# Performance work log

Hardware: AMD Instinct MI355X
Metric: run time of the kernel (lower is better)

Reference implementation:

```python
import jax, jax.numpy as jnp
import numpy as np

NUM_NODES = 10000
NUM_FEAT = 32
HIDDEN = 64
OUT_FEAT = 16
NUM_EDGES = 160000
SEQ_LEN = 12
BATCH = 1


def _gcn_conv(x, W, b, row, col, n):
    # PyG GCNConv: h = D^-1/2 (A+I) D^-1/2 (x @ W) + b
    # x: (n, T, F_in), row/col: (E+n,) with self-loops already appended
    h = x @ W                                              # (n, T, H)
    deg = jax.ops.segment_sum(jnp.ones_like(col, dtype=h.dtype), col, num_segments=n)
    dis = 1.0 / jnp.sqrt(jnp.maximum(deg, 1.0))            # deg >= 1 due to self-loops
    norm = dis[row] * dis[col]                             # (E+n,)
    msg = h[row] * norm[:, None, None]                     # gather + scale
    return jax.ops.segment_sum(msg, col, num_segments=n) + b


def _lstm_layer(x, wih, whh, bih, bhh):
    # x: (N, T, F); PyTorch gate order i, f, g, o
    H = whh.shape[1]
    Nn = x.shape[0]
    bias = bih + bhh

    def step(carry, xt):
        h, c = carry
        g = xt @ wih.T + h @ whh.T + bias
        i, f, gg, o = jnp.split(g, 4, axis=-1)
        c = jax.nn.sigmoid(f) * c + jax.nn.sigmoid(i) * jnp.tanh(gg)
        h = jax.nn.sigmoid(o) * jnp.tanh(c)
        return (h, c), h

    h0 = jnp.zeros((Nn, H), x.dtype)
    c0 = jnp.zeros((Nn, H), x.dtype)
    _, ys = jax.lax.scan(step, (h0, c0), jnp.transpose(x, (1, 0, 2)))
    return jnp.transpose(ys, (1, 0, 2))                    # (N, T, H)


def setup_inputs() -> dict:
    key = jax.random.key(0)
    ks = jax.random.split(key, 16)
    s_in = 1.0 / np.sqrt(NUM_FEAT)
    s_h = 1.0 / np.sqrt(HIDDEN)
    inp = {
        "x": jax.random.normal(ks[0], (BATCH, SEQ_LEN, NUM_NODES, NUM_FEAT), jnp.float32),
        "edge_index": jax.random.randint(ks[1], (2, NUM_EDGES), 0, NUM_NODES, dtype=jnp.int64),
        "gw0": jax.random.normal(ks[2], (NUM_FEAT, HIDDEN), jnp.float32) * s_in,
        "gb0": jnp.zeros((HIDDEN,), jnp.float32),
        "gw1": jax.random.normal(ks[3], (HIDDEN, HIDDEN), jnp.float32) * s_h,
        "gb1": jnp.zeros((HIDDEN,), jnp.float32),
        "wih0": jax.random.normal(ks[4], (4 * HIDDEN, HIDDEN), jnp.float32) * s_h,
        "whh0": jax.random.normal(ks[5], (4 * HIDDEN, HIDDEN), jnp.float32) * s_h,
        "bih0": jax.random.normal(ks[6], (4 * HIDDEN,), jnp.float32) * s_h,
        "bhh0": jax.random.normal(ks[7], (4 * HIDDEN,), jnp.float32) * s_h,
        "wih1": jax.random.normal(ks[8], (4 * HIDDEN, HIDDEN), jnp.float32) * s_h,
        "whh1": jax.random.normal(ks[9], (4 * HIDDEN, HIDDEN), jnp.float32) * s_h,
        "bih1": jax.random.normal(ks[10], (4 * HIDDEN,), jnp.float32) * s_h,
        "bhh1": jax.random.normal(ks[11], (4 * HIDDEN,), jnp.float32) * s_h,
        "fc_w": jax.random.normal(ks[12], (OUT_FEAT, HIDDEN), jnp.float32) * s_h,
        "fc_b": jnp.zeros((OUT_FEAT,), jnp.float32),
    }
    return inp


def reference(x, edge_index, gw0, gb0, gw1, gb1, wih0, whh0, bih0, bhh0,
              wih1, whh1, bih1, bhh1, fc_w, fc_b):
    B, T, n, F = x.shape
    BN = B * n
    # (B, T, N, F) -> (B, N, T, F) -> (B*N, T, F); the per-timestep GCN loop in
    # the original is batched over T here (same math, edge_index is time-invariant).
    xs = jnp.transpose(x, (0, 2, 1, 3)).reshape(BN, T, F)
    loops = jnp.arange(BN, dtype=edge_index.dtype)
    row = jnp.concatenate([edge_index[0], loops])
    col = jnp.concatenate([edge_index[1], loops])
    h = jax.nn.relu(_gcn_conv(xs, gw0, gb0, row, col, BN))
    h = jax.nn.relu(_gcn_conv(h, gw1, gb1, row, col, BN))
    h = _lstm_layer(h, wih0, whh0, bih0, bhh0)
    h = _lstm_layer(h, wih1, whh1, bih1, bhh1)
    out = h[:, -1, :] @ fc_w.T + fc_b                      # last timestep only
    return out.reshape(B, n, OUT_FEAT)
```

## Files before the change

kernel.cpp:

```cpp
#include <hip/hip_runtime.h>
#include <hip/hip_bf16.h>

constexpr int kNN  = 10000;
constexpr int kTT  = 12;
constexpr int kFIN = 32;
constexpr int kHH  = 64;
constexpr int kH4  = 256;
constexpr int kOUT = 16;
constexpr int kNE  = 160000;

typedef _Float16 half8 __attribute__((ext_vector_type(8)));
typedef _Float16 half4 __attribute__((ext_vector_type(4)));
typedef _Float16 half2t __attribute__((ext_vector_type(2)));
typedef float floatx4 __attribute__((ext_vector_type(4)));

__device__ __forceinline__ float sigf(float x){ return 1.f/(1.f+__expf(-x)); }
__device__ __forceinline__ float tanh_fast(float x){
  float xc = fminf(fmaxf(x,-30.f),30.f);
  float e = __expf(-2.f*xc);
  return (1.f-e)/(1.f+e);
}

__global__ void k_detect(const int* __restrict__ ei, int* __restrict__ anyf){
  int a = 0;
  for (int i = blockIdx.x*256 + threadIdx.x; i < kNE; i += gridDim.x*256)
    a |= ei[2*i+1];
  unsigned long long m = __ballot(a != 0);
  if ((threadIdx.x & 63) == 0 && m) atomicOr(anyf, 1);
}

__global__ void k_deg(const int* __restrict__ ei, const int* __restrict__ anyf,
                      int* __restrict__ cnt){
  int e = blockIdx.x*256 + threadIdx.x;
  if (e >= kNE) return;
  int c = (anyf[0]==0) ? ei[2*(kNE+e)] : ei[kNE+e];
  atomicAdd(&cnt[c], 1);
}

__global__ void k_scan(const int* __restrict__ cnt, int* __restrict__ offs,
                       float* __restrict__ dis){
  __shared__ int part[256];
  int tid = threadIdx.x;
  const int CH = (kNN + 255)/256;
  int lo = tid*CH, hi = min(lo+CH, kNN);
  int s = 0;
  for (int i = lo; i < hi; ++i) s += cnt[i];
  part[tid] = s;
  __syncthreads();
  if (tid == 0){
    int run = 0;
    for (int i = 0; i < 256; ++i){ int v = part[i]; part[i] = run; run += v; }
  }
  __syncthreads();
  int run = part[tid];
  for (int i = lo; i < hi; ++i){ offs[i] = run; run += cnt[i]; }
  if (hi == kNN) offs[kNN] = run;
  for (int i = tid; i < kNN; i += 256) dis[i] = rsqrtf((float)(cnt[i]+1));
}

__global__ void k_scatter(const int* __restrict__ ei, const int* __restrict__ anyf,
                          const int* __restrict__ offs, int* __restrict__ cur,
                          const float* __restrict__ dis,
                          int* __restrict__ esrc, float* __restrict__ ew){
  int e = blockIdx.x*256 + threadIdx.x;
  if (e >= kNE) return;
  int f = (anyf[0]==0);
  int r = f ? ei[2*e]         : ei[e];
  int c = f ? ei[2*(kNE+e)]   : ei[kNE+e];
  int p = offs[c] + atomicAdd(&cur[c], 1);
  esrc[p] = r;
  ew[p] = dis[r]*dis[c];
}

template<int K, int N, typename TI>
__global__ __launch_bounds__(256) void k_gemm(const TI* __restrict__ in,
                      const float* __restrict__ Wg,
                      _Float16* __restrict__ out){
  constexpr int COLG = N/4;
  constexpr int ROWG = 256/COLG;
  constexpr int MR   = 4;
  constexpr int MTILE= ROWG*MR;
  constexpr int AP   = K + 4;
  __shared__ float Wl[K*N];
  __shared__ float Al[MTILE*AP];
  int tid = threadIdx.x;
  int m0 = blockIdx.x*MTILE;
  if constexpr (__is_same(TI, _Float16)){
    for (int idx = tid; idx < MTILE*K/8; idx += 256){
      int r = idx/(K/8), k8 = idx - r*(K/8);
      half8 v = *(const half8*)&in[(size_t)(m0 + r)*K + k8*8];
      float* dst = &Al[r*AP + k8*8];
      #pragma unroll
      for (int j = 0; j < 8; ++j) dst[j] = (float)v[j];
    }
  } else {
    for (int idx = tid; idx < MTILE*K/4; idx += 256){
      int r = idx/(K/4), k4 = idx - r*(K/4);
      float4 v = *(const float4*)&in[(size_t)(m0 + r)*K + k4*4];
      float* dst = &Al[r*AP + k4*4];
      dst[0]=v.x; dst[1]=v.y; dst[2]=v.z; dst[3]=v.w;
    }
  }
  for (int idx = tid; idx < K*N; idx += 256) Wl[idx] = Wg[idx];
  __syncthreads();
  int cg = tid % COLG, rg = tid / COLG;
  int c0 = cg*4, r0 = rg*MR;
  float acc[MR][4];
  #pragma unroll
  for (int r=0;r<MR;++r){acc[r][0]=0.f;acc[r][1]=0.f;acc[r][2]=0.f;acc[r][3]=0.f;}
  #pragma unroll 2
  for (int k = 0; k < K; k += 4){
    float4 wv[4];
    #pragma unroll
    for (int kk = 0; kk < 4; ++kk) wv[kk] = *(const float4*)&Wl[(k+kk)*N + c0];
    #pragma unroll
    for (int r = 0; r < MR; ++r){
      float4 a4 = *(const float4*)&Al[(r0+r)*AP + k];
      acc[r][0] = fmaf(a4.x, wv[0].x, acc[r][0]);
      acc[r][1] = fmaf(a4.x, wv[0].y, acc[r][1]);
      acc[r][2] = fmaf(a4.x, wv[0].z, acc[r][2]);
      acc[r][3] = fmaf(a4.x, wv[0].w, acc[r][3]);
      acc[r][0] = fmaf(a4.y, wv[1].x, acc[r][0]);
      acc[r][1] = fmaf(a4.y, wv[1].y, acc[r][1]);
      acc[r][2] = fmaf(a4.y, wv[1].z, acc[r][2]);
      acc[r][3] = fmaf(a4.y, wv[1].w, acc[r][3]);
      acc[r][0] = fmaf(a4.z, wv[2].x, acc[r][0]);
      acc[r][1] = fmaf(a4.z, wv[2].y, acc[r][1]);
      acc[r][2] = fmaf(a4.z, wv[2].z, acc[r][2]);
      acc[r][3] = fmaf(a4.z, wv[2].w, acc[r][3]);
      acc[r][0] = fmaf(a4.w, wv[3].x, acc[r][0]);
      acc[r][1] = fmaf(a4.w, wv[3].y, acc[r][1]);
      acc[r][2] = fmaf(a4.w, wv[3].z, acc[r][2]);
      acc[r][3] = fmaf(a4.w, wv[3].w, acc[r][3]);
    }
  }
  #pragma unroll
  for (int r = 0; r < MR; ++r){
    half4 hv;
    hv[0]=(_Float16)acc[r][0]; hv[1]=(_Float16)acc[r][1];
    hv[2]=(_Float16)acc[r][2]; hv[3]=(_Float16)acc[r][3];
    *(half4*)&out[(size_t)(m0 + r0 + r)*N + c0] = hv;
  }
}

template<bool TM>
__global__ __launch_bounds__(256) void k_agg(const _Float16* __restrict__ hin,
                     _Float16* __restrict__ hout,
                     const float* __restrict__ bias, const float* __restrict__ dis,
                     const int* __restrict__ offs, const int* __restrict__ esrc,
                     const float* __restrict__ ew){
  int wid = threadIdx.x >> 6, lane = threadIdx.x & 63;
  int gw = blockIdx.x*4 + wid;
  int tp = gw / kNN, n = gw - tp*kNN;
  int sel = lane >> 5, fp = lane & 31;
  int t = 2*tp + sel;
  const _Float16* hb = hin + (size_t)t*kNN*kHH;
  float d = dis[n], ws = d*d;
  half2t sv = *(const half2t*)&hb[(size_t)n*kHH + 2*fp];
  float a0 = ws*(float)sv[0], a1 = ws*(float)sv[1];
  int e0 = offs[n], e1 = offs[n+1];
  int e = e0;
  for (; e + 8 <= e1; e += 8){
    int s[8]; float w[8];
    #pragma unroll
    for (int u = 0; u < 8; ++u){ s[u] = esrc[e+u]; w[u] = ew[e+u]; }
    half2t v[8];
    #pragma unroll
    for (int u = 0; u < 8; ++u) v[u] = *(const half2t*)&hb[(size_t)s[u]*kHH + 2*fp];
    #pragma unroll
    for (int u = 0; u < 8; ++u){
      a0 = fmaf(w[u], (float)v[u][0], a0);
      a1 = fmaf(w[u], (float)v[u][1], a1);
    }
  }
  for (; e < e1; ++e){
    int su = esrc[e]; float wu = ew[e];
    half2t vu = *(const half2t*)&hb[(size_t)su*kHH + 2*fp];
    a0 = fmaf(wu, (float)vu[0], a0);
    a1 = fmaf(wu, (float)vu[1], a1);
  }
  a0 = fmaxf(a0 + bias[2*fp],   0.f);
  a1 = fmaxf(a1 + bias[2*fp+1], 0.f);
  half2t o; o[0] = (_Float16)a0; o[1] = (_Float16)a1;
  size_t oi = TM ? ((size_t)t*kNN + n)*kHH + 2*fp
                 : ((size_t)n*kTT + t)*kHH + 2*fp;
  *(half2t*)&hout[oi] = o;
}

__global__ __launch_bounds__(512) void k_rec2(const _Float16* __restrict__ xin,
                     const float* __restrict__ wih0, const float* __restrict__ whh0,
                     const float* __restrict__ bih0, const float* __restrict__ bhh0,
                     const float* __restrict__ wih1, const float* __restrict__ whh1,
                     const float* __restrict__ bih1, const float* __restrict__ bhh1,
                     const float* __restrict__ fcw, const float* __restrict__ fcb,
                     float* __restrict__ out){
  constexpr int LP = 72;
  __shared__ _Float16 h0b[2][16*LP];
  __shared__ _Float16 h1b[2][16*LP];
  int tid = threadIdx.x, w = tid >> 6, lane = tid & 63;
  int lo = lane & 15, hi4 = lane >> 4;
  int layer = w >> 2, wl = w & 3;
  int nb = blockIdx.x*16;

  const float* wih = layer ? wih1 : wih0;
  const float* whh = layer ? whh1 : whh0;
  const float* bi_ = layer ? bih1 : bih0;
  const float* bh_ = layer ? bhh1 : bhh0;

  half8 BI[4][2], BH[4][2];
  #pragma unroll
  for (int q = 0; q < 4; ++q){
    int row = q*kHH + wl*16 + lo;
    #pragma unroll
    for (int kt = 0; kt < 2; ++kt){
      const float* pi = wih + (size_t)row*kHH + kt*32 + hi4*8;
      const float* ph = whh + (size_t)row*kHH + kt*32 + hi4*8;
      half8 fi, fh;
      #pragma unroll
      for (int j = 0; j < 8; ++j){ fi[j] = (_Float16)pi[j]; fh[j] = (_Float16)ph[j]; }
      BI[q][kt] = fi; BH[q][kt] = fh;
    }
  }
  float bias[4];
  #pragma unroll
  for (int q = 0; q < 4; ++q){
    int col = q*kHH + wl*16 + lo;
    bias[q] = bi_[col] + bh_[col];
  }
  half8 FW[2];
  if (w == 4){
    #pragma unroll
    for (int kt = 0; kt < 2; ++kt){
      const float* pf = fcw + (size_t)lo*kHH + kt*32 + hi4*8;
      half8 f;
      #pragma unroll
      for (int j = 0; j < 8; ++j) f[j] = (_Float16)pf[j];
      FW[kt] = f;
    }
  }

  float c[4] = {0.f,0.f,0.f,0.f};
  half8 ax[2], ah[2], axn[2];

  const _Float16* xrow = xin + (size_t)(nb + lo)*kTT*kHH;
  if (layer == 0){
    #pragma unroll
    for (int kt = 0; kt < 2; ++kt) axn[kt] = *(const half8*)&xrow[kt*32 + hi4*8];
  }

  for (int i = 0; i < 13; ++i){
    int t = layer ? i-1 : i;
    bool act = layer ? (i >= 1) : (i < 12);
    if (act){
      if (layer == 0){
        ax[0] = axn[0]; ax[1] = axn[1];
        if (t < kTT-1){
          #pragma unroll
          for (int kt = 0; kt < 2; ++kt)
            axn[kt] = *(const half8*)&xrow[(size_t)(t+1)*kHH + kt*32 + hi4*8];
        }
      }
      floatx4 acc[4];
      #pragma unroll
      for (int q = 0; q < 4; ++q){
        floatx4 a = {0.f,0.f,0.f,0.f};
        a = __builtin_amdgcn_mfma_f32_16x16x32_f16(ax[0], BI[q][0], a, 0,0,0);
        a = __builtin_amdgcn_mfma_f32_16x16x32_f16(ax[1], BI[q][1], a, 0,0,0);
        acc[q] = a;
      }
      if (t > 0){
        #pragma unroll
        for (int q = 0; q < 4; ++q){
          floatx4 a = acc[q];
          a = __builtin_amdgcn_mfma_f32_16x16x32_f16(ah[0], BH[q][0], a, 0,0,0);
          a = __builtin_amdgcn_mfma_f32_16x16x32_f16(ah[1], BH[q][1], a, 0,0,0);
          acc[q] = a;
        }
      }
      _Float16* hb = layer ? &h1b[t & 1][0] : &h0b[t & 1][0];
      #pragma unroll
      for (int r = 0; r < 4; ++r){
        float gi = acc[0][r] + bias[0];
        float gf = acc[1][r] + bias[1];
        float gg = acc[2][r] + bias[2];
        float go = acc[3][r] + bias[3];
        float ii = sigf(gi), ff = sigf(gf), gt = tanh_fast(gg), oo = sigf(go);
        c[r] = ff*c[r] + ii*gt;
        float hn = oo * tanh_fast(c[r]);
        hb[(hi4*4 + r)*LP + wl*16 + lo] = (_Float16)hn;
      }
    }
    __syncthreads();
    if (layer == 0){
      if (i < 11){
        const _Float16* rb = &h0b[i & 1][0];
        #pragma unroll
        for (int kt = 0; kt < 2; ++kt)
          ah[kt] = *(const half8*)&rb[lo*LP + kt*32 + hi4*8];
      }
    } else {
      if (i < 12){
        const _Float16* rb = &h0b[i & 1][0];
        #pragma unroll
        for (int kt = 0; kt < 2; ++kt)
          ax[kt] = *(const half8*)&rb[lo*LP + kt*32 + hi4*8];
      }
      if (i >= 1 && i < 12){
        const _Float16* rb = &h1b[(i-1) & 1][0];
        #pragma unroll
        for (int kt = 0; kt < 2; ++kt)
          ah[kt] = *(const half8*)&rb[lo*LP + kt*32 + hi4*8];
      }
    }
  }
  if (w == 4){
    const _Float16* rb = &h1b[1][0];
    half8 a0 = *(const half8*)&rb[lo*LP + 0*32 + hi4*8];
    half8 a1 = *(const half8*)&rb[lo*LP + 1*32 + hi4*8];
    floatx4 a = {0.f,0.f,0.f,0.f};
    a = __builtin_amdgcn_mfma_f32_16x16x32_f16(a0, FW[0], a, 0,0,0);
    a = __builtin_amdgcn_mfma_f32_16x16x32_f16(a1, FW[1], a, 0,0,0);
    float bo = fcb[lo];
    #pragma unroll
    for (int r = 0; r < 4; ++r)
      out[(size_t)(nb + hi4*4 + r)*kOUT + lo] = a[r] + bo;
  }
}

extern "C" void kernel_launch(void* const* d_in, const int* in_sizes, int n_in,
                              void* d_out, int out_size, void* d_ws, size_t ws_size,
                              hipStream_t stream){
  const float* x    = (const float*)d_in[0];
  const int*   ei   = (const int*)  d_in[1];
  const float* gw0  = (const float*)d_in[2];
  const float* gb0  = (const float*)d_in[3];
  const float* gw1  = (const float*)d_in[4];
  const float* gb1  = (const float*)d_in[5];
  const float* wih0 = (const float*)d_in[6];
  const float* whh0 = (const float*)d_in[7];
  const float* bih0 = (const float*)d_in[8];
  const float* bhh0 = (const float*)d_in[9];
  const float* wih1 = (const float*)d_in[10];
  const float* whh1 = (const float*)d_in[11];
  const float* bih1 = (const float*)d_in[12];
  const float* bhh1 = (const float*)d_in[13];
  const float* fcw  = (const float*)d_in[14];
  const float* fcb  = (const float*)d_in[15];
  float* out = (float*)d_out;

  char* ws = (char*)d_ws;
  size_t p = 0;
  auto carve = [&](size_t bytes)->char*{
    char* r = ws + p;
    p += (bytes + 255) & ~(size_t)255;
    return r;
  };
  int*   anyf = (int*)  carve(256);
  int*   cnt  = (int*)  carve(sizeof(int)*kNN);
  int*   cur  = (int*)  carve(sizeof(int)*kNN);
  size_t zbytes = p;
  int*   offs = (int*)  carve(sizeof(int)*(kNN+1));
  float* dis  = (float*)carve(sizeof(float)*kNN);
  int*   esrc = (int*)  carve(sizeof(int)*kNE);
  float* ew   = (float*)carve(sizeof(float)*kNE);
  _Float16* bufA = (_Float16*)carve(sizeof(_Float16)*(size_t)kNN*kTT*kHH);
  _Float16* bufB = (_Float16*)carve(sizeof(_Float16)*(size_t)kNN*kTT*kHH);
  (void)ws_size; (void)in_sizes; (void)n_in; (void)out_size;

  hipMemsetAsync(ws, 0, zbytes, stream);
  k_detect <<<80, 256, 0, stream>>>(ei, anyf);
  k_deg    <<<(kNE+255)/256, 256, 0, stream>>>(ei, anyf, cnt);
  k_scan   <<<1, 256, 0, stream>>>(cnt, offs, dis);
  k_scatter<<<(kNE+255)/256, 256, 0, stream>>>(ei, anyf, offs, cur, dis, esrc, ew);

  k_gemm<kFIN, kHH, float><<<(kNN*kTT)/64, 256, 0, stream>>>(x, gw0, bufA);
  k_agg<true> <<<(kNN*kTT/2)/4, 256, 0, stream>>>(bufA, bufB, gb0, dis, offs, esrc, ew);
  k_gemm<kHH, kHH, _Float16><<<(kNN*kTT)/64, 256, 0, stream>>>(bufB, gw1, bufA);
  k_agg<false><<<(kNN*kTT/2)/4, 256, 0, stream>>>(bufA, bufB, gb1, dis, offs, esrc, ew);

  k_rec2<<<kNN/16, 512, 0, stream>>>(bufB, wih0, whh0, bih0, bhh0,
                                     wih1, whh1, bih1, bhh1, fcw, fcb, out);
}
```

Measured before the change: 343.4 us.

## Aggregate before transform in GCN, pack edge data, batch two tiles per LSTM block

Several changes land together. The first GCN layer now aggregates the 32-wide input before the matmul, which uses the linearity of A(XW) = (AX)W to cut gather width. Bias and ReLU move into the GEMM epilogue. Edge source and weight are packed into one int2, and the edge bounds are made wave-uniform with readfirstlane. Input x is cast to fp16 inside the detect kernel, the scan uses wave shuffles, and the LSTM kernel handles two 16-node tiles per block to amortise weight loads and sync. The risks are an extra fp16 rounding of x and fewer LSTM blocks (313), which lowers occupancy across CUs.

After: 328.3 us. 4.4% less time.

```diff
diff --git a/kernel.cpp b/kernel.cpp
--- a/kernel.cpp
+++ b/kernel.cpp
@@ -21,12 +21,20 @@
   return (1.f-e)/(1.f+e);
 }
 
-__global__ void k_detect(const int* __restrict__ ei, int* __restrict__ anyf){
+__global__ void k_detect_cast(const int* __restrict__ ei, int* __restrict__ anyf,
+                              const float* __restrict__ x, _Float16* __restrict__ xh){
   int a = 0;
   for (int i = blockIdx.x*256 + threadIdx.x; i < kNE; i += gridDim.x*256)
     a |= ei[2*i+1];
   unsigned long long m = __ballot(a != 0);
   if ((threadIdx.x & 63) == 0 && m) atomicOr(anyf, 1);
+  const int NV = kNN*kTT*kFIN/4;
+  for (int i = blockIdx.x*256 + threadIdx.x; i < NV; i += gridDim.x*256){
+    float4 v = *(const float4*)&x[4*i];
+    half4 h;
+    h[0]=(_Float16)v.x; h[1]=(_Float16)v.y; h[2]=(_Float16)v.z; h[3]=(_Float16)v.w;
+    *(half4*)&xh[4*i] = h;
+  }
 }
 
 __global__ void k_deg(const int* __restrict__ ei, const int* __restrict__ anyf,
@@ -39,20 +47,24 @@
 
 __global__ void k_scan(const int* __restrict__ cnt, int* __restrict__ offs,
                        float* __restrict__ dis){
-  __shared__ int part[256];
+  __shared__ int wsum[4];
   int tid = threadIdx.x;
   const int CH = (kNN + 255)/256;
   int lo = tid*CH, hi = min(lo+CH, kNN);
   int s = 0;
   for (int i = lo; i < hi; ++i) s += cnt[i];
-  part[tid] = s;
+  int orig = s;
+  int lane = tid & 63, wv = tid >> 6;
+  #pragma unroll
+  for (int d = 1; d < 64; d <<= 1){
+    int v = __shfl_up(s, d, 64);
+    if (lane >= d) s += v;
+  }
+  if (lane == 63) wsum[wv] = s;
   __syncthreads();
-  if (tid == 0){
-    int run = 0;
-    for (int i = 0; i < 256; ++i){ int v = part[i]; part[i] = run; run += v; }
-  }
-  __syncthreads();
-  int run = part[tid];
+  int add = 0;
+  for (int k2 = 0; k2 < wv; ++k2) add += wsum[k2];
+  int run = s - orig + add;
   for (int i = lo; i < hi; ++i){ offs[i] = run; run += cnt[i]; }
   if (hi == kNN) offs[kNN] = run;
   for (int i = tid; i < kNN; i += 256) dis[i] = rsqrtf((float)(cnt[i]+1));
@@ -61,20 +73,63 @@
 __global__ void k_scatter(const int* __restrict__ ei, const int* __restrict__ anyf,
                           const int* __restrict__ offs, int* __restrict__ cur,
                           const float* __restrict__ dis,
-                          int* __restrict__ esrc, float* __restrict__ ew){
+                          int2* __restrict__ edat){
   int e = blockIdx.x*256 + threadIdx.x;
   if (e >= kNE) return;
   int f = (anyf[0]==0);
   int r = f ? ei[2*e]         : ei[e];
   int c = f ? ei[2*(kNE+e)]   : ei[kNE+e];
   int p = offs[c] + atomicAdd(&cur[c], 1);
-  esrc[p] = r;
-  ew[p] = dis[r]*dis[c];
-}
-
-template<int K, int N, typename TI>
-__global__ __launch_bounds__(256) void k_gemm(const TI* __restrict__ in,
-                      const float* __restrict__ Wg,
+  edat[p] = make_int2(r, __float_as_int(dis[r]*dis[c]));
+}
+
+template<int F>
+__global__ __launch_bounds__(256) void k_agg(const _Float16* __restrict__ hin,
+                     _Float16* __restrict__ hout,
+                     const float* __restrict__ dis,
+                     const int* __restrict__ offs, const int2* __restrict__ edat){
+  constexpr int LPF = F/2;
+  constexpr int TPW = 64/LPF;
+  int wid = threadIdx.x >> 6, lane = threadIdx.x & 63;
+  int gw = blockIdx.x*4 + wid;
+  int tq = gw / kNN, n = gw - tq*kNN;
+  int fp = lane & (LPF-1), tsub = lane / LPF;
+  int t = TPW*tq + tsub;
+  const _Float16* hb = hin + (size_t)t*kNN*F;
+  float d = dis[n], ws = d*d;
+  half2t sv = *(const half2t*)&hb[(size_t)n*F + 2*fp];
+  float a0 = ws*(float)sv[0], a1 = ws*(float)sv[1];
+  int e0 = __builtin_amdgcn_readfirstlane(offs[n]);
+  int e1 = __builtin_amdgcn_readfirstlane(offs[n+1]);
+  int e = e0;
+  for (; e + 8 <= e1; e += 8){
+    int2 d8[8];
+    #pragma unroll
+    for (int u = 0; u < 8; ++u) d8[u] = edat[e+u];
+    half2t v[8];
+    #pragma unroll
+    for (int u = 0; u < 8; ++u) v[u] = *(const half2t*)&hb[(size_t)d8[u].x*F + 2*fp];
+    #pragma unroll
+    for (int u = 0; u < 8; ++u){
+      float wu = __int_as_float(d8[u].y);
+      a0 = fmaf(wu, (float)v[u][0], a0);
+      a1 = fmaf(wu, (float)v[u][1], a1);
+    }
+  }
+  for (; e < e1; ++e){
+    int2 du = edat[e];
+    float wu = __int_as_float(du.y);
+    half2t vu = *(const half2t*)&hb[(size_t)du.x*F + 2*fp];
+    a0 = fmaf(wu, (float)vu[0], a0);
+    a1 = fmaf(wu, (float)vu[1], a1);
+  }
+  half2t o; o[0] = (_Float16)a0; o[1] = (_Float16)a1;
+  *(half2t*)&hout[((size_t)t*kNN + n)*F + 2*fp] = o;
+}
+
+template<int K, int N, bool NM>
+__global__ __launch_bounds__(256) void k_gemm(const _Float16* __restrict__ in,
+                      const float* __restrict__ Wg, const float* __restrict__ bias,
                       _Float16* __restrict__ out){
   constexpr int COLG = N/4;
   constexpr int ROWG = 256/COLG;
@@ -85,21 +140,12 @@
   __shared__ float Al[MTILE*AP];
   int tid = threadIdx.x;
   int m0 = blockIdx.x*MTILE;
-  if constexpr (__is_same(TI, _Float16)){
-    for (int idx = tid; idx < MTILE*K/8; idx += 256){
-      int r = idx/(K/8), k8 = idx - r*(K/8);
-      half8 v = *(const half8*)&in[(size_t)(m0 + r)*K + k8*8];
-      float* dst = &Al[r*AP + k8*8];
-      #pragma unroll
-      for (int j = 0; j < 8; ++j) dst[j] = (float)v[j];
-    }
-  } else {
-    for (int idx = tid; idx < MTILE*K/4; idx += 256){
-      int r = idx/(K/4), k4 = idx - r*(K/4);
-      float4 v = *(const float4*)&in[(size_t)(m0 + r)*K + k4*4];
-      float* dst = &Al[r*AP + k4*4];
-      dst[0]=v.x; dst[1]=v.y; dst[2]=v.z; dst[3]=v.w;
-    }
+  for (int idx = tid; idx < MTILE*K/8; idx += 256){
+    int r = idx/(K/8), k8 = idx - r*(K/8);
+    half8 v = *(const half8*)&in[(size_t)(m0 + r)*K + k8*8];
+    float* dst = &Al[r*AP + k8*8];
+    #pragma unroll
+    for (int j = 0; j < 8; ++j) dst[j] = (float)v[j];
   }
   for (int idx = tid; idx < K*N; idx += 256) Wl[idx] = Wg[idx];
   __syncthreads();
@@ -134,57 +180,20 @@
       acc[r][3] = fmaf(a4.w, wv[3].w, acc[r][3]);
     }
   }
+  float4 bb = *(const float4*)&bias[c0];
   #pragma unroll
   for (int r = 0; r < MR; ++r){
     half4 hv;
-    hv[0]=(_Float16)acc[r][0]; hv[1]=(_Float16)acc[r][1];
-    hv[2]=(_Float16)acc[r][2]; hv[3]=(_Float16)acc[r][3];
-    *(half4*)&out[(size_t)(m0 + r0 + r)*N + c0] = hv;
-  }
-}
-
-template<bool TM>
-__global__ __launch_bounds__(256) void k_agg(const _Float16* __restrict__ hin,
-                     _Float16* __restrict__ hout,
-                     const float* __restrict__ bias, const float* __restrict__ dis,
-                     const int* __restrict__ offs, const int* __restrict__ esrc,
-                     const float* __restrict__ ew){
-  int wid = threadIdx.x >> 6, lane = threadIdx.x & 63;
-  int gw = blockIdx.x*4 + wid;
-  int tp = gw / kNN, n = gw - tp*kNN;
-  int sel = lane >> 5, fp = lane & 31;
-  int t = 2*tp + sel;
-  const _Float16* hb = hin + (size_t)t*kNN*kHH;
-  float d = dis[n], ws = d*d;
-  half2t sv = *(const half2t*)&hb[(size_t)n*kHH + 2*fp];
-  float a0 = ws*(float)sv[0], a1 = ws*(float)sv[1];
-  int e0 = offs[n], e1 = offs[n+1];
-  int e = e0;
-  for (; e + 8 <= e1; e += 8){
-    int s[8]; float w[8];
-    #pragma unroll
-    for (int u = 0; u < 8; ++u){ s[u] = esrc[e+u]; w[u] = ew[e+u]; }
-    half2t v[8];
-    #pragma unroll
-    for (int u = 0; u < 8; ++u) v[u] = *(const half2t*)&hb[(size_t)s[u]*kHH + 2*fp];
-    #pragma unroll
-    for (int u = 0; u < 8; ++u){
-      a0 = fmaf(w[u], (float)v[u][0], a0);
-      a1 = fmaf(w[u], (float)v[u][1], a1);
-    }
-  }
-  for (; e < e1; ++e){
-    int su = esrc[e]; float wu = ew[e];
-    half2t vu = *(const half2t*)&hb[(size_t)su*kHH + 2*fp];
-    a0 = fmaf(wu, (float)vu[0], a0);
-    a1 = fmaf(wu, (float)vu[1], a1);
-  }
-  a0 = fmaxf(a0 + bias[2*fp],   0.f);
-  a1 = fmaxf(a1 + bias[2*fp+1], 0.f);
-  half2t o; o[0] = (_Float16)a0; o[1] = (_Float16)a1;
-  size_t oi = TM ? ((size_t)t*kNN + n)*kHH + 2*fp
-                 : ((size_t)n*kTT + t)*kHH + 2*fp;
-  *(half2t*)&hout[oi] = o;
+    hv[0]=(_Float16)fmaxf(acc[r][0]+bb.x, 0.f);
+    hv[1]=(_Float16)fmaxf(acc[r][1]+bb.y, 0.f);
+    hv[2]=(_Float16)fmaxf(acc[r][2]+bb.z, 0.f);
+    hv[3]=(_Float16)fmaxf(acc[r][3]+bb.w, 0.f);
+    int m = m0 + r0 + r;
+    size_t oi;
+    if (NM){ int t = m/kNN, n = m - t*kNN; oi = ((size_t)n*kTT + t)*N + c0; }
+    else    oi = (size_t)m*N + c0;
+    *(half4*)&out[oi] = hv;
+  }
 }
 
 __global__ __launch_bounds__(512) void k_rec2(const _Float16* __restrict__ xin,
@@ -195,12 +204,12 @@
                      const float* __restrict__ fcw, const float* __restrict__ fcb,
                      float* __restrict__ out){
   constexpr int LP = 72;
-  __shared__ _Float16 h0b[2][16*LP];
-  __shared__ _Float16 h1b[2][16*LP];
+  __shared__ _Float16 h0b[2][2][16*LP];
+  __shared__ _Float16 h1b[2][2][16*LP];
   int tid = threadIdx.x, w = tid >> 6, lane = tid & 63;
   int lo = lane & 15, hi4 = lane >> 4;
   int layer = w >> 2, wl = w & 3;
-  int nb = blockIdx.x*16;
+  int nb0 = blockIdx.x*32;
 
   const float* wih = layer ? wih1 : wih0;
   const float* whh = layer ? whh1 : whh0;
@@ -228,7 +237,7 @@
     bias[q] = bi_[col] + bh_[col];
   }
   half8 FW[2];
-  if (w == 4){
+  if (w == 4 || w == 5){
     #pragma unroll
     for (int kt = 0; kt < 2; ++kt){
       const float* pf = fcw + (size_t)lo*kHH + kt*32 + hi4*8;
@@ -239,82 +248,103 @@
     }
   }
 
-  float c[4] = {0.f,0.f,0.f,0.f};
-  half8 ax[2], ah[2], axn[2];
-
-  const _Float16* xrow = xin + (size_t)(nb + lo)*kTT*kHH;
+  float c[2][4];
+  #pragma unroll
+  for (int u = 0; u < 2; ++u){c[u][0]=0.f;c[u][1]=0.f;c[u][2]=0.f;c[u][3]=0.f;}
+  half8 ax[2][2], ah[2][2], axn[2][2];
+
+  const _Float16* xrow[2];
+  #pragma unroll
+  for (int u = 0; u < 2; ++u)
+    xrow[u] = xin + (size_t)min(nb0 + u*16 + lo, kNN-1)*kTT*kHH;
   if (layer == 0){
     #pragma unroll
-    for (int kt = 0; kt < 2; ++kt) axn[kt] = *(const half8*)&xrow[kt*32 + hi4*8];
+    for (int u = 0; u < 2; ++u)
+      #pragma unroll
+      for (int kt = 0; kt < 2; ++kt)
+        axn[u][kt] = *(const half8*)&xrow[u][kt*32 + hi4*8];
   }
 
   for (int i = 0; i < 13; ++i){
     int t = layer ? i-1 : i;
     bool act = layer ? (i >= 1) : (i < 12);
     if (act){
-      if (layer == 0){
-        ax[0] = axn[0]; ax[1] = axn[1];
-        if (t < kTT-1){
-          #pragma unroll
-          for (int kt = 0; kt < 2; ++kt)
-            axn[kt] = *(const half8*)&xrow[(size_t)(t+1)*kHH + kt*32 + hi4*8];
-        }
-      }
-      floatx4 acc[4];
       #pragma unroll
-      for (int q = 0; q < 4; ++q){
-        floatx4 a = {0.f,0.f,0.f,0.f};
-        a = __builtin_amdgcn_mfma_f32_16x16x32_f16(ax[0], BI[q][0], a, 0,0,0);
-        a = __builtin_amdgcn_mfma_f32_16x16x32_f16(ax[1], BI[q][1], a, 0,0,0);
-        acc[q] = a;
-      }
-      if (t > 0){
+      for (int u = 0; u < 2; ++u){
+        if (layer == 0){
+          ax[u][0] = axn[u][0]; ax[u][1] = axn[u][1];
+          if (t < kTT-1){
+            #pragma unroll
+            for (int kt = 0; kt < 2; ++kt)
+              axn[u][kt] = *(const half8*)&xrow[u][(size_t)(t+1)*kHH + kt*32 + hi4*8];
+          }
+        }
+        floatx4 acc[4];
         #pragma unroll
         for (int q = 0; q < 4; ++q){
-          floatx4 a = acc[q];
-          a = __builtin_amdgcn_mfma_f32_16x16x32_f16(ah[0], BH[q][0], a, 0,0,0);
-          a = __builtin_amdgcn_mfma_f32_16x16x32_f16(ah[1], BH[q][1], a, 0,0,0);
+          floatx4 a = {0.f,0.f,0.f,0.f};
+          a = __builtin_amdgcn_mfma_f32_16x16x32_f16(ax[u][0], BI[q][0], a, 0,0,0);
+          a = __builtin_amdgcn_mfma_f32_16x16x32_f16(ax[u][1], BI[q][1], a, 0,0,0);
           acc[q] = a;
         }
-      }
-      _Float16* hb = layer ? &h1b[t & 1][0] : &h0b[t & 1][0];
-      #pragma unroll
-      for (int r = 0; r < 4; ++r){
-        float gi = acc[0][r] + bias[0];
-        float gf = acc[1][r] + bias[1];
-        float gg = acc[2][r] + bias[2];
-        float go = acc[3][r] + bias[3];
-        float ii = sigf(gi), ff = sigf(gf), gt = tanh_fast(gg), oo = sigf(go);
-        c[r] = ff*c[r] + ii*gt;
-        float hn = oo * tanh_fast(c[r]);
-        hb[(hi4*4 + r)*LP + wl*16 + lo] = (_Float16)hn;
+        if (t > 0){
+          #pragma unroll
+          for (int q = 0; q < 4; ++q){
+            floatx4 a = acc[q];
+            a = __builtin_amdgcn_mfma_f32_16x16x32_f16(ah[u][0], BH[q][0], a, 0,0,0);
+            a = __builtin_amdgcn_mfma_f32_16x16x32_f16(ah[u][1], BH[q][1], a, 0,0,0);
+            acc[q] = a;
+          }
+        }
+        _Float16* hb = layer ? &h1b[u][t & 1][0] : &h0b[u][t & 1][0];
+        #pragma unroll
+        for (int r = 0; r < 4; ++r){
+          float gi = acc[0][r] + bias[0];
+          float gf = acc[1][r] + bias[1];
+          float gg = acc[2][r] + bias[2];
+          float go = acc[3][r] + bias[3];
+          float ii = sigf(gi), ff = sigf(gf), gt = tanh_fast(gg), oo = sigf(go);
+          c[u][r] = ff*c[u][r] + ii*gt;
+          float hn = oo * tanh_fast(c[u][r]);
+          hb[(hi4*4 + r)*LP + wl*16 + lo] = (_Float16)hn;
+        }
       }
     }
     __syncthreads();
     if (layer == 0){
       if (i < 11){
-        const _Float16* rb = &h0b[i & 1][0];
         #pragma unroll
-        for (int kt = 0; kt < 2; ++kt)
-          ah[kt] = *(const half8*)&rb[lo*LP + kt*32 + hi4*8];
+        for (int u = 0; u < 2; ++u){
+          const _Float16* rb = &h0b[u][i & 1][0];
+          #pragma unroll
+          for (int kt = 0; kt < 2; ++kt)
+            ah[u][kt] = *(const half8*)&rb[lo*LP + kt*32 + hi4*8];
+        }
       }
     } else {
       if (i < 12){
-        const _Float16* rb = &h0b[i & 1][0];
         #pragma unroll
-        for (int kt = 0; kt < 2; ++kt)
-          ax[kt] = *(const half8*)&rb[lo*LP + kt*32 + hi4*8];
+        for (int u = 0; u < 2; ++u){
+          const _Float16* rb = &h0b[u][i & 1][0];
+          #pragma unroll
+          for (int kt = 0; kt < 2; ++kt)
+            ax[u][kt] = *(const half8*)&rb[lo*LP + kt*32 + hi4*8];
+        }
       }
       if (i >= 1 && i < 12){
-        const _Float16* rb = &h1b[(i-1) & 1][0];
         #pragma unroll
-        for (int kt = 0; kt < 2; ++kt)
-          ah[kt] = *(const half8*)&rb[lo*LP + kt*32 + hi4*8];
+        for (int u = 0; u < 2; ++u){
+          const _Float16* rb = &h1b[u][(i-1) & 1][0];
+          #pragma unroll
+          for (int kt = 0; kt < 2; ++kt)
+            ah[u][kt] = *(const half8*)&rb[lo*LP + kt*32 + hi4*8];
+        }
       }
     }
   }
-  if (w == 4){
-    const _Float16* rb = &h1b[1][0];
+  if (w == 4 || w == 5){
+    int u = w - 4;
+    const _Float16* rb = &h1b[u][1][0];
     half8 a0 = *(const half8*)&rb[lo*LP + 0*32 + hi4*8];
     half8 a1 = *(const half8*)&rb[lo*LP + 1*32 + hi4*8];
     floatx4 a = {0.f,0.f,0.f,0.f};
@@ -322,8 +352,10 @@
     a = __builtin_amdgcn_mfma_f32_16x16x32_f16(a1, FW[1], a, 0,0,0);
     float bo = fcb[lo];
     #pragma unroll
-    for (int r = 0; r < 4; ++r)
-      out[(size_t)(nb + hi4*4 + r)*kOUT + lo] = a[r] + bo;
+    for (int r = 0; r < 4; ++r){
+      int n = nb0 + u*16 + hi4*4 + r;
+      if (n < kNN) out[(size_t)n*kOUT + lo] = a[r] + bo;
+    }
   }
 }
 
@@ -361,23 +393,24 @@
   size_t zbytes = p;
   int*   offs = (int*)  carve(sizeof(int)*(kNN+1));
   float* dis  = (float*)carve(sizeof(float)*kNN);
-  int*   esrc = (int*)  carve(sizeof(int)*kNE);
-  float* ew   = (float*)carve(sizeof(float)*kNE);
+  int2*  edat = (int2*) carve(sizeof(int2)*kNE);
+  _Float16* xh   = (_Float16*)carve(sizeof(_Float16)*(size_t)kNN*kTT*kFIN);
+  _Float16* aggX = (_Float16*)carve(sizeof(_Float16)*(size_t)kNN*kTT*kFIN);
   _Float16* bufA = (_Float16*)carve(sizeof(_Float16)*(size_t)kNN*kTT*kHH);
   _Float16* bufB = (_Float16*)carve(sizeof(_Float16)*(size_t)kNN*kTT*kHH);
   (void)ws_size; (void)in_sizes; (void)n_in; (void)out_size;
 
   hipMemsetAsync(ws, 0, zbytes, stream);
-  k_detect <<<80, 256, 0, stream>>>(ei, anyf);
+  k_detect_cast<<<120, 256, 0, stream>>>(ei, anyf, x, xh);
   k_deg    <<<(kNE+255)/256, 256, 0, stream>>>(ei, anyf, cnt);
   k_scan   <<<1, 256, 0, stream>>>(cnt, offs, dis);
-  k_scatter<<<(kNE+255)/256, 256, 0, stream>>>(ei, anyf, offs, cur, dis, esrc, ew);
-
-  k_gemm<kFIN, kHH, float><<<(kNN*kTT)/64, 256, 0, stream>>>(x, gw0, bufA);
-  k_agg<true> <<<(kNN*kTT/2)/4, 256, 0, stream>>>(bufA, bufB, gb0, dis, offs, esrc, ew);
-  k_gemm<kHH, kHH, _Float16><<<(kNN*kTT)/64, 256, 0, stream>>>(bufB, gw1, bufA);
-  k_agg<false><<<(kNN*kTT/2)/4, 256, 0, stream>>>(bufA, bufB, gb1, dis, offs, esrc, ew);
-
-  k_rec2<<<kNN/16, 512, 0, stream>>>(bufB, wih0, whh0, bih0, bhh0,
-                                     wih1, whh1, bih1, bhh1, fcw, fcb, out);
-}
+  k_scatter<<<(kNE+255)/256, 256, 0, stream>>>(ei, anyf, offs, cur, dis, edat);
+
+  k_agg<kFIN><<<(kNN*(kTT/4))/4, 256, 0, stream>>>(xh, aggX, dis, offs, edat);
+  k_gemm<kFIN, kHH, false><<<(kNN*kTT)/64, 256, 0, stream>>>(aggX, gw0, gb0, bufB);
+  k_agg<kHH><<<(kNN*(kTT/2))/4, 256, 0, stream>>>(bufB, bufA, dis, offs, edat);
+  k_gemm<kHH, kHH, true><<<(kNN*kTT)/64, 256, 0, stream>>>(bufA, gw1, gb1, bufB);
+
+  k_rec2<<<(kNN+31)/32, 512, 0, stream>>>(bufB, wih0, whh0, bih0, bhh0,
+                                          wih1, whh1, bih1, bhh1, fcw, fcb, out);
+}
```
